# Optimization experiments

Hardware: AMD Instinct MI355X
Metric: run time of the kernel (lower is better)

The kernel has to match this reference:

```python
import jax, jax.numpy as jnp
import numpy as np

B, S, H = 2, 2048, 2048
NH, NKV, HD = 16, 4, 128
EPS = 1e-6


def setup_inputs() -> dict:
    key = jax.random.key(0)
    ks = jax.random.split(key, 8)
    s = 0.02
    x = jax.random.normal(ks[0], (B, S, H), dtype=jnp.float32)
    # real rotary tables: cos/sin of shape [S, HD]
    inv_freq = 1.0 / (10000.0 ** (np.arange(0, HD, 2, dtype=np.float32) / HD))
    t = np.arange(S, dtype=np.float32)
    freqs = np.outer(t, inv_freq)              # [S, HD/2]
    emb = np.concatenate([freqs, freqs], axis=-1)  # [S, HD]
    rotary_cos = jnp.asarray(np.cos(emb))
    rotary_sin = jnp.asarray(np.sin(emb))
    Wq = jax.random.normal(ks[1], (H, NH * HD), dtype=jnp.float32) * s
    Wk = jax.random.normal(ks[2], (H, NKV * HD), dtype=jnp.float32) * s
    Wv = jax.random.normal(ks[3], (H, NKV * HD), dtype=jnp.float32) * s
    Wo = jax.random.normal(ks[4], (H, H), dtype=jnp.float32) * s
    q_norm_w = jnp.ones((HD,), dtype=jnp.float32)
    k_norm_w = jnp.ones((HD,), dtype=jnp.float32)
    return {"x": x, "rotary_cos": rotary_cos, "rotary_sin": rotary_sin,
            "Wq": Wq, "Wk": Wk, "Wv": Wv, "Wo": Wo,
            "q_norm_w": q_norm_w, "k_norm_w": k_norm_w}


def _rms_norm(x, w):
    return x * jax.lax.rsqrt(jnp.mean(x * x, axis=-1, keepdims=True) + EPS) * w


def _rotate_half(x):
    half = x.shape[-1] // 2
    return jnp.concatenate([-x[..., half:], x[..., :half]], axis=-1)


def reference(x, rotary_cos, rotary_sin, Wq, Wk, Wv, Wo, q_norm_w, k_norm_w):
    b, s, _ = x.shape
    q = (x @ Wq).reshape(b, s, NH, HD)
    k = (x @ Wk).reshape(b, s, NKV, HD)
    v = (x @ Wv).reshape(b, s, NKV, HD)
    q = _rms_norm(q, q_norm_w)
    k = _rms_norm(k, k_norm_w)
    cos = rotary_cos[None, :, None, :]  # [1,S,1,HD]
    sin = rotary_sin[None, :, None, :]
    q = q * cos + _rotate_half(q) * sin
    k = k * cos + _rotate_half(k) * sin
    # GQA: repeat kv heads
    rep = NH // NKV
    k = jnp.repeat(k, rep, axis=2)  # [b,s,NH,HD]
    v = jnp.repeat(v, rep, axis=2)
    scores = jnp.einsum('bqhd,bkhd->bhqk', q, k) / jnp.sqrt(jnp.float32(HD))
    causal = jnp.tril(jnp.ones((s, s), dtype=bool))
    scores = jnp.where(causal[None, None], scores, -jnp.inf)
    probs = jax.nn.softmax(scores.astype(jnp.float32), axis=-1).astype(q.dtype)
    y = jnp.einsum('bhqk,bkhd->bqhd', probs, v).reshape(b, s, NH * HD)
    return y @ Wo
```

## Files before the change

### kernel.cpp

```cpp
#include <hip/hip_runtime.h>


#define S_LEN 2048

typedef __bf16 bf16_t;
typedef bf16_t bf16x8 __attribute__((ext_vector_type(8)));
typedef float f32x4 __attribute__((ext_vector_type(4)));
typedef float f32x16 __attribute__((ext_vector_type(16)));
typedef unsigned int u32x4 __attribute__((ext_vector_type(4)));
typedef unsigned short u16x4 __attribute__((ext_vector_type(4)));

__device__ __forceinline__ unsigned short f2bf(float f) {
  unsigned int u = __builtin_bit_cast(unsigned int, f);
  u += 0x7fffu + ((u >> 16) & 1u);
  return (unsigned short)(u >> 16);
}
__device__ __forceinline__ float bf2f(unsigned short h) {
  return __builtin_bit_cast(float, (unsigned int)h << 16);
}
__device__ __forceinline__ unsigned pk2(float a, float b) {
  return (unsigned)f2bf(a) | ((unsigned)f2bf(b) << 16);
}
__device__ __forceinline__ unsigned cvtpk(float a, float b) {
  unsigned r;
  asm("v_cvt_pk_bf16_f32 %0, %1, %2" : "=v"(r) : "v"(a), "v"(b));
  return r;
}

typedef const __attribute__((address_space(1))) unsigned int* gas1_t;
typedef __attribute__((address_space(3))) unsigned int* las3_t;
__device__ __forceinline__ void async16(const void* g, void* l) {
  __builtin_amdgcn_global_load_lds((gas1_t)g, (las3_t)l, 16, 0, 0);
}

__device__ __forceinline__ bf16x8 ldfrag(const void* p) {
  return __builtin_bit_cast(bf16x8, *(const u32x4*)p);
}
__device__ __forceinline__ f32x16 mfma32(bf16x8 a, bf16x8 b, f32x16 c) {
  return __builtin_amdgcn_mfma_f32_32x32x16_bf16(a, b, c, 0, 0, 0);
}
__device__ __forceinline__ f32x16 zero16() {
  f32x16 v;
#pragma unroll
  for (int i = 0; i < 16; i++) v[i] = 0.f;
  return v;
}

__global__ __launch_bounds__(256) void cast_x_kernel(
    const float* __restrict__ in, unsigned short* __restrict__ out, int n8) {
  int i = blockIdx.x * 256 + threadIdx.x;
  if (i >= n8) return;
  const f32x4* p = (const f32x4*)in + (size_t)i * 2;
  f32x4 a = p[0], b = p[1];
  u32x4 o;
  o.x = pk2(a.x, a.y);
  o.y = pk2(a.z, a.w);
  o.z = pk2(b.x, b.y);
  o.w = pk2(b.z, b.w);
  *(u32x4*)(out + (size_t)i * 8) = o;
}

__global__ __launch_bounds__(256) void transpose_cast_kernel(
    const float* __restrict__ in, unsigned short* __restrict__ out,
    int R, int C, int out_row_off, int out_ld) {
  __shared__ unsigned short L[64][68];
  int t = threadIdx.x;
  int r0 = blockIdx.y * 64, c0 = blockIdx.x * 64;
#pragma unroll
  for (int i = 0; i < 4; i++) {
    int r = i * 16 + (t >> 4);
    int c = (t & 15) * 4;
    f32x4 v = *(const f32x4*)&in[(size_t)(r0 + r) * C + c0 + c];
    u16x4 u;
    u.x = f2bf(v.x); u.y = f2bf(v.y); u.z = f2bf(v.z); u.w = f2bf(v.w);
    *(u16x4*)&L[r][c] = u;
  }
  __syncthreads();
#pragma unroll
  for (int i = 0; i < 4; i++) {
    int oc = i * 16 + (t >> 4);
    int orr = (t & 15) * 4;
    u16x4 u;
    u.x = L[orr + 0][oc]; u.y = L[orr + 1][oc];
    u.z = L[orr + 2][oc]; u.w = L[orr + 3][oc];
    *(u16x4*)&out[(size_t)(c0 + oc + out_row_off) * out_ld + r0 + orr] = u;
  }
}

__global__ __launch_bounds__(256) void gemm_bf16_kernel(
    const unsigned short* __restrict__ A, const unsigned short* __restrict__ Bt,
    void* __restrict__ Cout, int M, int N, int K, int out_bf16) {
  __shared__ unsigned short As[2][128 * 32];
  __shared__ unsigned short Bs[2][128 * 32];
  const int t = threadIdx.x, w = t >> 6, l = t & 63;
  const int wr = w >> 1, wc = w & 1;
  const int lrow = l & 15, lhi = l >> 4;
  const int row0 = blockIdx.y * 128, col0 = blockIdx.x * 128;
  const unsigned short* Ab = A + (size_t)row0 * K;
  const unsigned short* Bb = Bt + (size_t)col0 * K;
  const int srow = w * 32 + (l >> 2);
  const int scol = (l & 3) * 8;
  f32x4 z = {0.f, 0.f, 0.f, 0.f};
  f32x4 acc[4][4];
#pragma unroll
  for (int m = 0; m < 4; m++)
#pragma unroll
    for (int n = 0; n < 4; n++) acc[m][n] = z;

#define STAGE_G(tt, buf)                                                        \
  {                                                                             \
    const int k0_ = (tt) * 32;                                                  \
    async16(Ab + (size_t)srow * K + k0_ + scol,        &As[buf][(w * 32) * 32]);\
    async16(Ab + (size_t)(srow + 16) * K + k0_ + scol, &As[buf][(w * 32 + 16) * 32]); \
    async16(Bb + (size_t)srow * K + k0_ + scol,        &Bs[buf][(w * 32) * 32]);\
    async16(Bb + (size_t)(srow + 16) * K + k0_ + scol, &Bs[buf][(w * 32 + 16) * 32]); \
  }

  STAGE_G(0, 0);
  const int NT = K >> 5;
  for (int tt = 0; tt < NT; tt++) {
    const int cur = tt & 1;
    if (tt + 1 < NT) {
      STAGE_G(tt + 1, cur ^ 1);
      asm volatile("s_waitcnt vmcnt(4)" ::: "memory");
    } else {
      asm volatile("s_waitcnt vmcnt(0)" ::: "memory");
    }
    __builtin_amdgcn_s_barrier();
    __builtin_amdgcn_sched_barrier(0);
    bf16x8 af[4], bfr[4];
#pragma unroll
    for (int m = 0; m < 4; m++)
      af[m] = ldfrag(&As[cur][(wr * 64 + m * 16 + lrow) * 32 + lhi * 8]);
#pragma unroll
    for (int n = 0; n < 4; n++)
      bfr[n] = ldfrag(&Bs[cur][(wc * 64 + n * 16 + lrow) * 32 + lhi * 8]);
    __builtin_amdgcn_s_setprio(1);
#pragma unroll
    for (int m = 0; m < 4; m++)
#pragma unroll
      for (int n = 0; n < 4; n++)
        acc[m][n] = __builtin_amdgcn_mfma_f32_16x16x32_bf16(af[m], bfr[n], acc[m][n], 0, 0, 0);
    __builtin_amdgcn_s_setprio(0);
    __builtin_amdgcn_sched_barrier(0);
    __builtin_amdgcn_s_barrier();
  }
#undef STAGE_G

  if (out_bf16) {
    unsigned short* C = (unsigned short*)Cout;
#pragma unroll
    for (int m = 0; m < 4; m++)
#pragma unroll
      for (int n = 0; n < 4; n++)
#pragma unroll
        for (int r = 0; r < 4; r++) {
          size_t grow = row0 + wr * 64 + m * 16 + lhi * 4 + r;
          size_t gcol = col0 + wc * 64 + n * 16 + lrow;
          C[grow * N + gcol] = f2bf(acc[m][n][r]);
        }
  } else {
    float* C = (float*)Cout;
#pragma unroll
    for (int m = 0; m < 4; m++)
#pragma unroll
      for (int n = 0; n < 4; n++)
#pragma unroll
        for (int r = 0; r < 4; r++) {
          size_t grow = row0 + wr * 64 + m * 16 + lhi * 4 + r;
          size_t gcol = col0 + wc * 64 + n * 16 + lrow;
          C[grow * N + gcol] = acc[m][n][r];
        }
  }
}

__global__ __launch_bounds__(256) void mid_kernel(
    const unsigned short* __restrict__ QKV, const float* __restrict__ cosT,
    const float* __restrict__ sinT, const float* __restrict__ qw,
    const float* __restrict__ kw, unsigned short* __restrict__ Qpk,
    unsigned short* __restrict__ Kpk, unsigned short* __restrict__ Vpk) {
  int w = threadIdx.x >> 6, l = threadIdx.x & 63;
  int g = blockIdx.x * 4 + w;
  int bs = g / 24, idx = g - bs * 24;
  int b = bs >> 11, s = bs & 2047;
  int d0 = 2 * l;
  unsigned int uu = *(const unsigned int*)(QKV + (size_t)bs * 3072 + idx * 128 + d0);
  float x0 = bf2f((unsigned short)(uu & 0xffffu));
  float x1 = bf2f((unsigned short)(uu >> 16));
  if (idx < 20) {
    const float* nw = (idx < 16) ? qw : kw;
    float ss = x0 * x0 + x1 * x1;
#pragma unroll
    for (int mk = 1; mk < 64; mk <<= 1) ss += __shfl_xor(ss, mk);
    float inv = rsqrtf(ss * (1.0f / 128.0f) + 1e-6f);
    float n0 = x0 * inv * nw[d0], n1 = x1 * inv * nw[d0 + 1];
    float p0 = __shfl_xor(n0, 32), p1 = __shfl_xor(n1, 32);
    float sg = (l < 32) ? -1.0f : 1.0f;
    float c0 = cosT[s * 128 + d0], c1 = cosT[s * 128 + d0 + 1];
    float sn0 = sinT[s * 128 + d0], sn1 = sinT[s * 128 + d0 + 1];
    float o0 = n0 * c0 + sg * p0 * sn0;
    float o1 = n1 * c1 + sg * p1 * sn1;
    int mf = d0 >> 4, hi = (d0 >> 3) & 1, j = d0 & 7;
    int blk = s >> 5, r31 = s & 31;
    int foff = (mf * 2 + hi) * 256 + r31 * 8 + j;
    unsigned short* dst;
    if (idx < 16) {
      const float qs = 0.08838834764831845f * 1.4426950408889634f;
      o0 *= qs; o1 *= qs;
      dst = Qpk + (((size_t)(b * 16 + idx)) * 64 + blk) * 4096 + foff;
    } else {
      dst = Kpk + (((size_t)(b * 4 + (idx - 16))) * 64 + blk) * 4096 + foff;
    }
    *(unsigned int*)dst = pk2(o0, o1);
  } else {
    int kvh = idx - 20;
    int kv0 = s >> 6, ks = (s >> 4) & 3, his = (s >> 3) & 1, j = s & 7;
    int n = d0 >> 5, d31 = d0 & 31;
    size_t base = (((size_t)(b * 4 + kvh)) * 32 + kv0) * 8192 +
                  (((n * 4 + ks) * 2 + his) * 256 + d31 * 8 + j);
    Vpk[base] = f2bf(x0);
    Vpk[base + 8] = f2bf(x1);
  }
}

__global__ __launch_bounds__(256) void attn_kernel(
    const unsigned short* __restrict__ Qpk, const unsigned short* __restrict__ Kpk,
    const unsigned short* __restrict__ Vpk, unsigned short* __restrict__ Y) {
  __shared__ unsigned short Ks[2][2][8192];
  __shared__ unsigned short Vs[2][2][8192];
  const int w = threadIdx.x >> 6, l = threadIdx.x & 63;
  const int q31 = l & 31, hi = l >> 5;
  const int bid = blockIdx.x;
  const int xcd = bid & 7;
  const int b = xcd >> 2, kvh = xcd & 3;
  const int h = kvh * 4 + w;
  const int bh = b * 16 + h;
  const int pj = bid >> 3;
  const unsigned short* Kg = Kpk + (size_t)(b * 4 + kvh) * 262144;
  const unsigned short* Vg = Vpk + (size_t)(b * 4 + kvh) * 262144;

#define STAGE_SUB(ti, buf, sub)                                                \
  {                                                                            \
    const unsigned short* kg_ = Kg + (size_t)(ti) * 8192;                      \
    const unsigned short* vg_ = Vg + (size_t)(ti) * 8192;                      \
    _Pragma("unroll")                                                          \
    for (int i_ = 0; i_ < 4; i_++) {                                           \
      int seg_ = i_ * 4 + w;                                                   \
      async16(kg_ + (size_t)(seg_ * 64 + l) * 8, &Ks[buf][sub][seg_ * 512]);   \
      async16(vg_ + (size_t)(seg_ * 64 + l) * 8, &Vs[buf][sub][seg_ * 512]);   \
    }                                                                          \
  }

  for (int phase = 0; phase < 2; phase++) {
    const int strip = phase ? pj : (63 - pj);
    const int q0w = strip * 32;
    const int qg = q0w + q31;
    const unsigned short* Qs =
        Qpk + (((size_t)bh * 64 + strip) * 4096) + (size_t)l * 8;

    bf16x8 qf[8];
#pragma unroll
    for (int mf = 0; mf < 8; mf++)
      qf[mf] = ldfrag(Qs + mf * 512);
    asm volatile("s_waitcnt vmcnt(0)" ::: "memory");

    const int nt = (q0w + 95) >> 6;
    const int nr = (nt + 1) >> 1;
    STAGE_SUB(0, 0, 0);
    STAGE_SUB((nt > 1 ? 1 : 0), 0, 1);

    f32x16 o[4];
#pragma unroll
    for (int n = 0; n < 4; n++) o[n] = zero16();
    float m = -3.0e38f, lsum = 0.f;

    for (int r = 0; r < nr; r++) {
      const int cur = r & 1;
      if (r + 1 < nr) {
        const int t0 = 2 * r + 2;
        const int t1 = (2 * r + 3 < nt) ? (2 * r + 3) : (nt - 1);
        STAGE_SUB(t0, cur ^ 1, 0);
        STAGE_SUB(t1, cur ^ 1, 1);
        asm volatile("s_waitcnt vmcnt(16)" ::: "memory");
      } else {
        asm volatile("s_waitcnt vmcnt(0)" ::: "memory");
      }
      __builtin_amdgcn_s_barrier();
      __builtin_amdgcn_sched_barrier(0);

#pragma unroll
      for (int sub = 0; sub < 2; sub++) {
        const int ti = 2 * r + sub;
        if (ti < nt) {
          const int kv0 = ti << 6;
          f32x16 s0 = zero16(), s1 = zero16();
          const unsigned short* kt = &Ks[cur][sub][0];
          __builtin_amdgcn_s_setprio(1);
#pragma unroll
          for (int mf = 0; mf < 8; mf++) {
            s0 = mfma32(ldfrag(kt + mf * 512 + l * 8), qf[mf], s0);
            s1 = mfma32(ldfrag(kt + 4096 + mf * 512 + l * 8), qf[mf], s1);
          }
          __builtin_amdgcn_s_setprio(0);
          if (ti == nt - 1) {
            const int kvb = kv0 + 4 * hi;
#pragma unroll
            for (int rr = 0; rr < 16; rr++) {
              int kv = kvb + (rr & 3) + 8 * (rr >> 2);
              if (kv > qg) s0[rr] = -3.0e38f;
              if (kv + 32 > qg) s1[rr] = -3.0e38f;
            }
          }
          float pm = s0[0];
#pragma unroll
          for (int rr = 1; rr < 16; rr++) pm = fmaxf(pm, s0[rr]);
#pragma unroll
          for (int rr = 0; rr < 16; rr++) pm = fmaxf(pm, s1[rr]);
          pm = fmaxf(pm, __shfl_xor(pm, 32));
          if (__any(pm > m + 8.0f)) {
            float mn = fmaxf(m, pm);
            float scl = exp2f(m - mn);
            m = mn;
            lsum *= scl;
#pragma unroll
            for (int rr = 0; rr < 16; rr++) {
              float sr = __shfl(scl, (rr & 3) + 8 * (rr >> 2) + 4 * hi);
              o[0][rr] *= sr; o[1][rr] *= sr; o[2][rr] *= sr; o[3][rr] *= sr;
            }
          }
#pragma unroll
          for (int rr = 0; rr < 16; rr++) {
            s0[rr] = exp2f(s0[rr] - m);
            s1[rr] = exp2f(s1[rr] - m);
          }
          float ts = 0.f;
#pragma unroll
          for (int rr = 0; rr < 16; rr++) ts += s0[rr] + s1[rr];
          ts += __shfl_xor(ts, 32);
          lsum += ts;
          bf16x8 paf[4];
#pragma unroll
          for (int blk = 0; blk < 2; blk++) {
            f32x16& sx = blk ? s1 : s0;
#pragma unroll
            for (int blk2 = 0; blk2 < 2; blk2++) {
              const int base = 8 * blk2;
              unsigned g00 = cvtpk(sx[base + 0], sx[base + 1]);
              unsigned g01 = cvtpk(sx[base + 2], sx[base + 3]);
              unsigned g10 = cvtpk(sx[base + 4], sx[base + 5]);
              unsigned g11 = cvtpk(sx[base + 6], sx[base + 7]);
              unsigned snd0 = hi ? g00 : g10;
              unsigned snd1 = hi ? g01 : g11;
              unsigned r0 = (unsigned)__shfl_xor((int)snd0, 32);
              unsigned r1 = (unsigned)__shfl_xor((int)snd1, 32);
              unsigned own0 = hi ? g10 : g00;
              unsigned own1 = hi ? g11 : g01;
              u32x4 wv;
              wv.x = hi ? r0 : own0;
              wv.y = hi ? r1 : own1;
              wv.z = hi ? own0 : r0;
              wv.w = hi ? own1 : r1;
              paf[blk * 2 + blk2] = __builtin_bit_cast(bf16x8, wv);
            }
          }
          const unsigned short* vt = &Vs[cur][sub][0];
          __builtin_amdgcn_s_setprio(1);
#pragma unroll
          for (int n = 0; n < 4; n++) {
#pragma unroll
            for (int ks = 0; ks < 4; ks++)
              o[n] = mfma32(paf[ks], ldfrag(vt + (n * 4 + ks) * 512 + l * 8), o[n]);
          }
          __builtin_amdgcn_s_setprio(0);
        }
      }

      __builtin_amdgcn_sched_barrier(0);
      __builtin_amdgcn_s_barrier();
    }
    float linv = 1.0f / lsum;
#pragma unroll
    for (int rr = 0; rr < 16; rr++) {
      int cr = (rr & 3) + 8 * (rr >> 2) + 4 * hi;
      float lr = __shfl(linv, cr);
      int qrow = q0w + cr;
      size_t rowoff = ((size_t)(b * S_LEN + qrow)) * 2048 + h * 128 + q31;
      Y[rowoff]      = f2bf(o[0][rr] * lr);
      Y[rowoff + 32] = f2bf(o[1][rr] * lr);
      Y[rowoff + 64] = f2bf(o[2][rr] * lr);
      Y[rowoff + 96] = f2bf(o[3][rr] * lr);
    }
  }
#undef STAGE_SUB
}

extern "C" void kernel_launch(void* const* d_in, const int* in_sizes, int n_in,
                              void* d_out, int out_size, void* d_ws, size_t ws_size,
                              hipStream_t stream) {
  const float* x  = (const float*)d_in[0];
  const float* rc = (const float*)d_in[1];
  const float* rs = (const float*)d_in[2];
  const float* Wq = (const float*)d_in[3];
  const float* Wk = (const float*)d_in[4];
  const float* Wv = (const float*)d_in[5];
  const float* Wo = (const float*)d_in[6];
  const float* qw = (const float*)d_in[7];
  const float* kw = (const float*)d_in[8];
  float* out = (float*)d_out;
  char* ws = (char*)d_ws;

  unsigned short* xb   = (unsigned short*)(ws + 0);
  unsigned short* WT   = (unsigned short*)(ws + 16777216);
  unsigned short* WoT  = (unsigned short*)(ws + 29360128);
  unsigned short* QKVb = (unsigned short*)(ws + 37748736);
  unsigned short* Qpk  = (unsigned short*)(ws + 0);
  unsigned short* Kpk  = (unsigned short*)(ws + 16777216);
  unsigned short* Vpk  = (unsigned short*)(ws + 20971520);
  unsigned short* Yb   = (unsigned short*)(ws + 37748736);

  cast_x_kernel<<<4096, 256, 0, stream>>>(x, xb, 1048576);
  transpose_cast_kernel<<<dim3(32, 32), 256, 0, stream>>>(Wq, WT, 2048, 2048, 0, 2048);
  transpose_cast_kernel<<<dim3(8, 32), 256, 0, stream>>>(Wk, WT, 2048, 512, 2048, 2048);
  transpose_cast_kernel<<<dim3(8, 32), 256, 0, stream>>>(Wv, WT, 2048, 512, 2560, 2048);
  transpose_cast_kernel<<<dim3(32, 32), 256, 0, stream>>>(Wo, WoT, 2048, 2048, 0, 2048);
  gemm_bf16_kernel<<<dim3(24, 32), 256, 0, stream>>>(xb, WT, QKVb, 4096, 3072, 2048, 1);
  mid_kernel<<<24576, 256, 0, stream>>>(QKVb, rc, rs, qw, kw, Qpk, Kpk, Vpk);
  attn_kernel<<<256, 256, 0, stream>>>(Qpk, Kpk, Vpk, Yb);
  gemm_bf16_kernel<<<dim3(16, 32), 256, 0, stream>>>(Yb, WoT, out, 4096, 2048, 2048, 0);
}
```

Before: 242.2 us.

## Split attention KV range across two wave groups with LDS merge of partial softmax

Doubles the attention block to 512 threads: two groups of four waves each process half of the causal KV tiles for the same query strip, using 32-wide KV tiles with a triple-buffered LDS pipeline. The V packing in mid_kernel changes to the matching 32-row tile layout. At the end, the per-row max and sum are exchanged through LDS and the partial outputs are combined by a flash-decoding style merge. The aim is to raise wave-level parallelism and latency hiding per CU, at the cost of extra barriers, the LDS reduction and a larger LDS footprint that may limit occupancy.

After: 224.9 us. -7.2%, faster.

```diff
diff --git a/kernel.cpp b/kernel.cpp
--- a/kernel.cpp
+++ b/kernel.cpp
@@ -214,40 +214,43 @@
     *(unsigned int*)dst = pk2(o0, o1);
   } else {
     int kvh = idx - 20;
-    int kv0 = s >> 6, ks = (s >> 4) & 3, his = (s >> 3) & 1, j = s & 7;
+    int blk = s >> 5, ks = (s >> 4) & 1, his = (s >> 3) & 1, j = s & 7;
     int n = d0 >> 5, d31 = d0 & 31;
-    size_t base = (((size_t)(b * 4 + kvh)) * 32 + kv0) * 8192 +
-                  (((n * 4 + ks) * 2 + his) * 256 + d31 * 8 + j);
+    size_t base = (((size_t)(b * 4 + kvh)) * 64 + blk) * 4096 +
+                  (((n * 2 + ks) * 2 + his) * 256 + d31 * 8 + j);
     Vpk[base] = f2bf(x0);
     Vpk[base + 8] = f2bf(x1);
   }
 }
 
-__global__ __launch_bounds__(256) void attn_kernel(
+__global__ __launch_bounds__(512) void attn_kernel(
     const unsigned short* __restrict__ Qpk, const unsigned short* __restrict__ Kpk,
     const unsigned short* __restrict__ Vpk, unsigned short* __restrict__ Y) {
-  __shared__ unsigned short Ks[2][2][8192];
-  __shared__ unsigned short Vs[2][2][8192];
-  const int w = threadIdx.x >> 6, l = threadIdx.x & 63;
+  __shared__ __attribute__((aligned(16))) unsigned char lds_raw[100352];
+  const int t = threadIdx.x, w = t >> 6, l = t & 63;
   const int q31 = l & 31, hi = l >> 5;
+  const int grp = w >> 2, hw = w & 3;
   const int bid = blockIdx.x;
   const int xcd = bid & 7;
   const int b = xcd >> 2, kvh = xcd & 3;
-  const int h = kvh * 4 + w;
-  const int bh = b * 16 + h;
+  const int hd = kvh * 4 + hw;
+  const int bh = b * 16 + hd;
   const int pj = bid >> 3;
   const unsigned short* Kg = Kpk + (size_t)(b * 4 + kvh) * 262144;
   const unsigned short* Vg = Vpk + (size_t)(b * 4 + kvh) * 262144;
-
-#define STAGE_SUB(ti, buf, sub)                                                \
+  float* mlb = (float*)(lds_raw + 98304);
+
+#define STAGE1(st, buf)                                                        \
   {                                                                            \
-    const unsigned short* kg_ = Kg + (size_t)(ti) * 8192;                      \
-    const unsigned short* vg_ = Vg + (size_t)(ti) * 8192;                      \
+    unsigned char* base_ = lds_raw + ((buf) * 2 + grp) * 16384;                \
+    const unsigned short* kg_ = Kg + (size_t)(st) * 4096;                      \
+    const unsigned short* vg_ = Vg + (size_t)(st) * 4096;                      \
     _Pragma("unroll")                                                          \
     for (int i_ = 0; i_ < 4; i_++) {                                           \
-      int seg_ = i_ * 4 + w;                                                   \
-      async16(kg_ + (size_t)(seg_ * 64 + l) * 8, &Ks[buf][sub][seg_ * 512]);   \
-      async16(vg_ + (size_t)(seg_ * 64 + l) * 8, &Vs[buf][sub][seg_ * 512]);   \
+      int c_ = hw * 4 + i_;                                                    \
+      const unsigned short* src_ = (c_ < 8) ? (kg_ + c_ * 512 + l * 8)         \
+                                            : (vg_ + (c_ - 8) * 512 + l * 8);  \
+      async16(src_, base_ + c_ * 1024 + l * 16);                               \
     }                                                                          \
   }
 
@@ -255,143 +258,149 @@
     const int strip = phase ? pj : (63 - pj);
     const int q0w = strip * 32;
     const int qg = q0w + q31;
-    const unsigned short* Qs =
-        Qpk + (((size_t)bh * 64 + strip) * 4096) + (size_t)l * 8;
-
+    const int nt = strip + 1;
+    const int hcut = (nt + 1) >> 1;
+    const int myFirst = grp ? hcut : 0;
+    const int myCnt = grp ? (nt - hcut) : hcut;
+    const int R = hcut;
+
+    const unsigned short* Qs = Qpk + (((size_t)bh * 64 + strip) * 4096) + (size_t)l * 8;
     bf16x8 qf[8];
 #pragma unroll
-    for (int mf = 0; mf < 8; mf++)
-      qf[mf] = ldfrag(Qs + mf * 512);
+    for (int mf = 0; mf < 8; mf++) qf[mf] = ldfrag(Qs + mf * 512);
     asm volatile("s_waitcnt vmcnt(0)" ::: "memory");
 
-    const int nt = (q0w + 95) >> 6;
-    const int nr = (nt + 1) >> 1;
-    STAGE_SUB(0, 0, 0);
-    STAGE_SUB((nt > 1 ? 1 : 0), 0, 1);
+    { int st0 = (myCnt > 0) ? myFirst : 0; STAGE1(st0, 0); }
 
     f32x16 o[4];
 #pragma unroll
     for (int n = 0; n < 4; n++) o[n] = zero16();
     float m = -3.0e38f, lsum = 0.f;
 
-    for (int r = 0; r < nr; r++) {
-      const int cur = r & 1;
-      if (r + 1 < nr) {
-        const int t0 = 2 * r + 2;
-        const int t1 = (2 * r + 3 < nt) ? (2 * r + 3) : (nt - 1);
-        STAGE_SUB(t0, cur ^ 1, 0);
-        STAGE_SUB(t1, cur ^ 1, 1);
-        asm volatile("s_waitcnt vmcnt(16)" ::: "memory");
-      } else {
-        asm volatile("s_waitcnt vmcnt(0)" ::: "memory");
-      }
+    for (int r = 0; r < R; r++) {
+      const int buf = r % 3;
+      { int st = (r + 1 < myCnt) ? (myFirst + r + 1) : 0; STAGE1(st, (r + 1) % 3); }
+      asm volatile("s_waitcnt vmcnt(4)" ::: "memory");
       __builtin_amdgcn_s_barrier();
       __builtin_amdgcn_sched_barrier(0);
 
-#pragma unroll
-      for (int sub = 0; sub < 2; sub++) {
-        const int ti = 2 * r + sub;
-        if (ti < nt) {
-          const int kv0 = ti << 6;
-          f32x16 s0 = zero16(), s1 = zero16();
-          const unsigned short* kt = &Ks[cur][sub][0];
-          __builtin_amdgcn_s_setprio(1);
-#pragma unroll
-          for (int mf = 0; mf < 8; mf++) {
-            s0 = mfma32(ldfrag(kt + mf * 512 + l * 8), qf[mf], s0);
-            s1 = mfma32(ldfrag(kt + 4096 + mf * 512 + l * 8), qf[mf], s1);
+      if (r < myCnt) {
+        const int ti = myFirst + r;
+        const int kv0 = ti << 5;
+        const unsigned short* base =
+            (const unsigned short*)(lds_raw + (buf * 2 + grp) * 16384);
+        f32x16 sA = zero16(), sB = zero16();
+        __builtin_amdgcn_s_setprio(1);
+#pragma unroll
+        for (int mf = 0; mf < 4; mf++) {
+          sA = mfma32(ldfrag(base + mf * 512 + l * 8), qf[mf], sA);
+          sB = mfma32(ldfrag(base + (mf + 4) * 512 + l * 8), qf[mf + 4], sB);
+        }
+        __builtin_amdgcn_s_setprio(0);
+#pragma unroll
+        for (int rr = 0; rr < 16; rr++) sA[rr] += sB[rr];
+        if (ti == nt - 1) {
+#pragma unroll
+          for (int rr = 0; rr < 16; rr++) {
+            int kv = kv0 + (rr & 3) + 8 * (rr >> 2) + 4 * hi;
+            if (kv > qg) sA[rr] = -3.0e38f;
           }
-          __builtin_amdgcn_s_setprio(0);
-          if (ti == nt - 1) {
-            const int kvb = kv0 + 4 * hi;
-#pragma unroll
-            for (int rr = 0; rr < 16; rr++) {
-              int kv = kvb + (rr & 3) + 8 * (rr >> 2);
-              if (kv > qg) s0[rr] = -3.0e38f;
-              if (kv + 32 > qg) s1[rr] = -3.0e38f;
-            }
+        }
+        float pm = sA[0];
+#pragma unroll
+        for (int rr = 1; rr < 16; rr++) pm = fmaxf(pm, sA[rr]);
+        pm = fmaxf(pm, __shfl_xor(pm, 32));
+        if (__any(pm > m + 8.0f)) {
+          float mn = fmaxf(m, pm);
+          float scl = exp2f(m - mn);
+          m = mn; lsum *= scl;
+#pragma unroll
+          for (int rr = 0; rr < 16; rr++) {
+            float sr = __shfl(scl, (rr & 3) + 8 * (rr >> 2) + 4 * hi);
+            o[0][rr] *= sr; o[1][rr] *= sr; o[2][rr] *= sr; o[3][rr] *= sr;
           }
-          float pm = s0[0];
-#pragma unroll
-          for (int rr = 1; rr < 16; rr++) pm = fmaxf(pm, s0[rr]);
-#pragma unroll
-          for (int rr = 0; rr < 16; rr++) pm = fmaxf(pm, s1[rr]);
-          pm = fmaxf(pm, __shfl_xor(pm, 32));
-          if (__any(pm > m + 8.0f)) {
-            float mn = fmaxf(m, pm);
-            float scl = exp2f(m - mn);
-            m = mn;
-            lsum *= scl;
-#pragma unroll
-            for (int rr = 0; rr < 16; rr++) {
-              float sr = __shfl(scl, (rr & 3) + 8 * (rr >> 2) + 4 * hi);
-              o[0][rr] *= sr; o[1][rr] *= sr; o[2][rr] *= sr; o[3][rr] *= sr;
-            }
-          }
-#pragma unroll
-          for (int rr = 0; rr < 16; rr++) {
-            s0[rr] = exp2f(s0[rr] - m);
-            s1[rr] = exp2f(s1[rr] - m);
-          }
-          float ts = 0.f;
-#pragma unroll
-          for (int rr = 0; rr < 16; rr++) ts += s0[rr] + s1[rr];
-          ts += __shfl_xor(ts, 32);
-          lsum += ts;
-          bf16x8 paf[4];
-#pragma unroll
-          for (int blk = 0; blk < 2; blk++) {
-            f32x16& sx = blk ? s1 : s0;
-#pragma unroll
-            for (int blk2 = 0; blk2 < 2; blk2++) {
-              const int base = 8 * blk2;
-              unsigned g00 = cvtpk(sx[base + 0], sx[base + 1]);
-              unsigned g01 = cvtpk(sx[base + 2], sx[base + 3]);
-              unsigned g10 = cvtpk(sx[base + 4], sx[base + 5]);
-              unsigned g11 = cvtpk(sx[base + 6], sx[base + 7]);
-              unsigned snd0 = hi ? g00 : g10;
-              unsigned snd1 = hi ? g01 : g11;
-              unsigned r0 = (unsigned)__shfl_xor((int)snd0, 32);
-              unsigned r1 = (unsigned)__shfl_xor((int)snd1, 32);
-              unsigned own0 = hi ? g10 : g00;
-              unsigned own1 = hi ? g11 : g01;
-              u32x4 wv;
-              wv.x = hi ? r0 : own0;
-              wv.y = hi ? r1 : own1;
-              wv.z = hi ? own0 : r0;
-              wv.w = hi ? own1 : r1;
-              paf[blk * 2 + blk2] = __builtin_bit_cast(bf16x8, wv);
-            }
-          }
-          const unsigned short* vt = &Vs[cur][sub][0];
-          __builtin_amdgcn_s_setprio(1);
-#pragma unroll
-          for (int n = 0; n < 4; n++) {
-#pragma unroll
-            for (int ks = 0; ks < 4; ks++)
-              o[n] = mfma32(paf[ks], ldfrag(vt + (n * 4 + ks) * 512 + l * 8), o[n]);
-          }
-          __builtin_amdgcn_s_setprio(0);
-        }
+        }
+#pragma unroll
+        for (int rr = 0; rr < 16; rr++) sA[rr] = exp2f(sA[rr] - m);
+        float ts = 0.f;
+#pragma unroll
+        for (int rr = 0; rr < 16; rr++) ts += sA[rr];
+        ts += __shfl_xor(ts, 32);
+        lsum += ts;
+        bf16x8 paf[2];
+#pragma unroll
+        for (int f = 0; f < 2; f++) {
+          const int bs8 = 8 * f;
+          unsigned g00 = cvtpk(sA[bs8 + 0], sA[bs8 + 1]);
+          unsigned g01 = cvtpk(sA[bs8 + 2], sA[bs8 + 3]);
+          unsigned g10 = cvtpk(sA[bs8 + 4], sA[bs8 + 5]);
+          unsigned g11 = cvtpk(sA[bs8 + 6], sA[bs8 + 7]);
+          unsigned snd0 = hi ? g00 : g10;
+          unsigned snd1 = hi ? g01 : g11;
+          unsigned r0 = (unsigned)__shfl_xor((int)snd0, 32);
+          unsigned r1 = (unsigned)__shfl_xor((int)snd1, 32);
+          unsigned own0 = hi ? g10 : g00;
+          unsigned own1 = hi ? g11 : g01;
+          u32x4 wv;
+          wv.x = hi ? r0 : own0;
+          wv.y = hi ? r1 : own1;
+          wv.z = hi ? own0 : r0;
+          wv.w = hi ? own1 : r1;
+          paf[f] = __builtin_bit_cast(bf16x8, wv);
+        }
+        __builtin_amdgcn_s_setprio(1);
+#pragma unroll
+        for (int n = 0; n < 4; n++) {
+          o[n] = mfma32(paf[0], ldfrag(base + 4096 + (n * 2 + 0) * 512 + l * 8), o[n]);
+          o[n] = mfma32(paf[1], ldfrag(base + 4096 + (n * 2 + 1) * 512 + l * 8), o[n]);
+        }
+        __builtin_amdgcn_s_setprio(0);
       }
-
-      __builtin_amdgcn_sched_barrier(0);
-      __builtin_amdgcn_s_barrier();
-    }
-    float linv = 1.0f / lsum;
+    }
+
+    __syncthreads();
+    if (l < 32) {
+      mlb[hw * 128 + grp * 64 + q31] = m;
+      mlb[hw * 128 + grp * 64 + 32 + q31] = lsum;
+    }
+    __syncthreads();
+    float m_o = mlb[hw * 128 + (grp ^ 1) * 64 + q31];
+    float l_o = mlb[hw * 128 + (grp ^ 1) * 64 + 32 + q31];
+    float M = fmaxf(m, m_o);
+    float sc = exp2f(m - M);
+    float lF = lsum * sc + l_o * exp2f(m_o - M);
 #pragma unroll
     for (int rr = 0; rr < 16; rr++) {
-      int cr = (rr & 3) + 8 * (rr >> 2) + 4 * hi;
-      float lr = __shfl(linv, cr);
-      int qrow = q0w + cr;
-      size_t rowoff = ((size_t)(b * S_LEN + qrow)) * 2048 + h * 128 + q31;
-      Y[rowoff]      = f2bf(o[0][rr] * lr);
-      Y[rowoff + 32] = f2bf(o[1][rr] * lr);
-      Y[rowoff + 64] = f2bf(o[2][rr] * lr);
-      Y[rowoff + 96] = f2bf(o[3][rr] * lr);
-    }
-  }
-#undef STAGE_SUB
+      float sr = __shfl(sc, (rr & 3) + 8 * (rr >> 2) + 4 * hi);
+      o[0][rr] *= sr; o[1][rr] *= sr; o[2][rr] *= sr; o[3][rr] *= sr;
+    }
+    float* ob = (float*)lds_raw + hw * 4096;
+    if (grp == 1) {
+#pragma unroll
+      for (int rr = 0; rr < 16; rr++) {
+        int cr = (rr & 3) + 8 * (rr >> 2) + 4 * hi;
+#pragma unroll
+        for (int n = 0; n < 4; n++) ob[cr * 128 + n * 32 + q31] = o[n][rr];
+      }
+    }
+    __syncthreads();
+    if (grp == 0) {
+      float linv = 1.0f / lF;
+#pragma unroll
+      for (int rr = 0; rr < 16; rr++) {
+        int cr = (rr & 3) + 8 * (rr >> 2) + 4 * hi;
+        float lr = __shfl(linv, cr);
+        int qrow = q0w + cr;
+        size_t rowoff = ((size_t)(b * S_LEN + qrow)) * 2048 + hd * 128 + q31;
+        Y[rowoff]      = f2bf((o[0][rr] + ob[cr * 128 + q31]) * lr);
+        Y[rowoff + 32] = f2bf((o[1][rr] + ob[cr * 128 + 32 + q31]) * lr);
+        Y[rowoff + 64] = f2bf((o[2][rr] + ob[cr * 128 + 64 + q31]) * lr);
+        Y[rowoff + 96] = f2bf((o[3][rr] + ob[cr * 128 + 96 + q31]) * lr);
+      }
+    }
+    __syncthreads();
+  }
+#undef STAGE1
 }
 
 extern "C" void kernel_launch(void* const* d_in, const int* in_sizes, int n_in,
@@ -425,6 +434,6 @@
   transpose_cast_kernel<<<dim3(32, 32), 256, 0, stream>>>(Wo, WoT, 2048, 2048, 0, 2048);
   gemm_bf16_kernel<<<dim3(24, 32), 256, 0, stream>>>(xb, WT, QKVb, 4096, 3072, 2048, 1);
   mid_kernel<<<24576, 256, 0, stream>>>(QKVb, rc, rs, qw, kw, Qpk, Kpk, Vpk);
-  attn_kernel<<<256, 256, 0, stream>>>(Qpk, Kpk, Vpk, Yb);
+  attn_kernel<<<256, 512, 0, stream>>>(Qpk, Kpk, Vpk, Yb);
   gemm_bf16_kernel<<<dim3(16, 32), 256, 0, stream>>>(Yb, WoT, out, 4096, 2048, 2048, 0);
 }
```
